# Kernel tuning notes

Measured on AMD Instinct MI355X. Metric: run time of the kernel, lower is better.

## Reference

```python
import jax, jax.numpy as jnp
import numpy as np

N, E, D, NUM_REL, NUM_LAYERS = 20000, 100000, 768, 7, 5  # 6 edge types + self-loop relation


def setup_inputs() -> dict:
    key = jax.random.key(0)
    ks = jax.random.split(key, 8)
    x = jax.random.normal(ks[0], (N, D), dtype=jnp.float32)
    edge_index = jax.random.randint(ks[1], (2, E), 0, N, dtype=jnp.int64)
    # original edge_type values are in [-1, 5]; module adds 1 -> [0, 6]
    edge_type = jax.random.randint(ks[2], (E,), -1, 6, dtype=jnp.int64)
    scale = 1.0 / np.sqrt(D)
    weights = jax.random.normal(ks[3], (NUM_LAYERS, NUM_REL, D, D), dtype=jnp.float32) * scale
    roots = jax.random.normal(ks[4], (NUM_LAYERS, D, D), dtype=jnp.float32) * scale
    biases = jax.random.normal(ks[5], (NUM_LAYERS, D), dtype=jnp.float32) * 0.01
    return {"x": x, "edge_index": edge_index, "edge_type": edge_type,
            "weights": weights, "roots": roots, "biases": biases}


def _rgcn_conv(h, src, dst, safe_et, W, root, b):
    # PyG RGCNConv (aggr='mean', root_weight=True, bias=True):
    #   out = x @ root + b + sum_r mean_{edges of rel r into v}(x[src]) @ W_r
    n = h.shape[0]
    hs = h[src]  # [E, D] gather once, reused across relations
    out = h @ root + b
    for r in range(NUM_REL):
        m = (safe_et == r).astype(h.dtype)  # [E]
        msg_sum = jax.ops.segment_sum(hs * m[:, None], dst, num_segments=n)  # [N, D]
        cnt = jax.ops.segment_sum(m, dst, num_segments=n)  # [N]
        mean = msg_sum / jnp.maximum(cnt, 1.0)[:, None]  # zero where no rel-r edges
        out = out + mean @ W[r]
    return out


def reference(x, edge_index, edge_type, weights, roots, biases):
    src, dst = edge_index[0], edge_index[1]
    safe_et = edge_type + 1  # [-1..5] -> [0..6]
    h = x
    for l in range(NUM_LAYERS):
        h = _rgcn_conv(h, src, dst, safe_et, weights[l], roots[l], biases[l])
        h = jax.nn.relu(h)  # dropout=0 -> identity
    return h
```

## Files before the change

kernel.cpp:

```cpp
#include <hip/hip_runtime.h>

typedef unsigned short u16;
typedef unsigned int   u32;
typedef __attribute__((ext_vector_type(8))) short short8;
typedef __attribute__((ext_vector_type(4))) float f32x4;

#define DD      768
#define KK      6144
#define NREL    7
#define NLAYERS 5

__device__ __forceinline__ float b2f(u16 v) {
  return __uint_as_float(((u32)v) << 16);
}
__device__ __forceinline__ u16 f2bf(float f) {
  u32 x = __float_as_uint(f);
  x += 0x7fffu + ((x >> 16) & 1u);
  return (u16)(x >> 16);
}
__device__ __forceinline__ void gload16(const void* g, void* l) {
  __builtin_amdgcn_global_load_lds(
      (const __attribute__((address_space(1))) void*)g,
      (__attribute__((address_space(3))) void*)l, 16, 0, 0);
}


__global__ void cast_x_kernel(const float* __restrict__ x, u16* __restrict__ H, size_t n) {
  for (size_t i = ((size_t)blockIdx.x * 256 + threadIdx.x) * 4; i < n; i += (size_t)gridDim.x * 256 * 4) {
    float4 v = *(const float4*)&x[i];
    u32 lo = (u32)f2bf(v.x) | ((u32)f2bf(v.y) << 16);
    u32 hi = (u32)f2bf(v.z) | ((u32)f2bf(v.w) << 16);
    uint2 o; o.x = lo; o.y = hi;
    *(uint2*)&H[i] = o;
  }
}

__global__ void count_kernel(const int* __restrict__ eidx, const int* __restrict__ etype,
                             int* cnt_dst, int* cnt_rel, int E, int Nn) {
  int e = blockIdx.x * 256 + threadIdx.x;
  if (e >= E) return;
  int dst = eidx[E + e];
  int rel = etype[e] + 1;
  atomicAdd(&cnt_dst[dst], 1);
  atomicAdd(&cnt_rel[(size_t)rel * Nn + dst], 1);
}

__global__ __launch_bounds__(1024) void scan_kernel(const int* __restrict__ cnt, int* __restrict__ offs, int n) {
  __shared__ int part[1024];
  int t = threadIdx.x;
  int per = (n + 1023) / 1024;
  int base = t * per;
  int s = 0;
  for (int i = 0; i < per; ++i) { int idx = base + i; if (idx < n) s += cnt[idx]; }
  part[t] = s;
  __syncthreads();
  for (int o = 1; o < 1024; o <<= 1) {
    int v = (t >= o) ? part[t - o] : 0;
    __syncthreads();
    part[t] += v;
    __syncthreads();
  }
  int excl = (t == 0) ? 0 : part[t - 1];
  s = excl;
  for (int i = 0; i < per; ++i) { int idx = base + i; if (idx < n) { offs[idx] = s; s += cnt[idx]; } }
  if (t == 1023) offs[n] = part[1023];
}

__global__ void fillperm_kernel(const int* __restrict__ eidx, const int* __restrict__ offs,
                                int* fill, int* perm, int E) {
  int e = blockIdx.x * 256 + threadIdx.x;
  if (e >= E) return;
  int dst = eidx[E + e];
  int pos = offs[dst] + atomicAdd(&fill[dst], 1);
  perm[pos] = e;
}

__global__ void wcat_kernel(const float* __restrict__ W, const float* __restrict__ R, u16* __restrict__ Bt) {
  __shared__ float t[32 * 33];
  int b = blockIdx.x;
  int s = b / 576, rem = b % 576;
  int kt = rem / 24, nt = rem % 24;
  const float* src = (s == 0) ? R : (W + (size_t)(s - 1) * DD * DD);
  int tj = threadIdx.x & 31, ti = threadIdx.x >> 5;
#pragma unroll
  for (int i = 0; i < 4; ++i) {
    int kk = kt * 32 + ti + i * 8;
    t[(ti + i * 8) * 33 + tj] = src[(size_t)kk * DD + nt * 32 + tj];
  }
  __syncthreads();
#pragma unroll
  for (int i = 0; i < 4; ++i) {
    int nn_ = nt * 32 + ti + i * 8;
    Bt[(size_t)nn_ * KK + (size_t)s * DD + kt * 32 + tj] = f2bf(t[tj * 33 + ti + i * 8]);
  }
}

__global__ __launch_bounds__(192) void aggregate_kernel(
    const u16* __restrict__ H, const int* __restrict__ esrc, const int* __restrict__ etype,
    const int* __restrict__ offs, const int* __restrict__ perm, const int* __restrict__ cnt_rel,
    u16* __restrict__ Acat, int node0, int Nn) {
  int v = node0 + blockIdx.x;
  int t = threadIdx.x;
  int j0 = t * 4;
  size_t rowbase = (size_t)blockIdx.x * KK;
  *(uint2*)&Acat[rowbase + j0] = *(const uint2*)&H[(size_t)v * DD + j0];
  float a0[4] = {0,0,0,0}, a1[4] = {0,0,0,0}, a2[4] = {0,0,0,0}, a3[4] = {0,0,0,0};
  float a4[4] = {0,0,0,0}, a5[4] = {0,0,0,0}, a6[4] = {0,0,0,0};
  int beg = offs[v], end = offs[v + 1];
  for (int e = beg; e < end; ++e) {
    int eid = perm[e];
    int src = esrc[eid];
    int rel = etype[eid] + 1;
    uint2 w = *(const uint2*)&H[(size_t)src * DD + j0];
    float f0 = b2f((u16)(w.x & 0xffff));
    float f1 = b2f((u16)(w.x >> 16));
    float f2 = b2f((u16)(w.y & 0xffff));
    float f3 = b2f((u16)(w.y >> 16));
    switch (rel) {
      case 0: a0[0]+=f0; a0[1]+=f1; a0[2]+=f2; a0[3]+=f3; break;
      case 1: a1[0]+=f0; a1[1]+=f1; a1[2]+=f2; a1[3]+=f3; break;
      case 2: a2[0]+=f0; a2[1]+=f1; a2[2]+=f2; a2[3]+=f3; break;
      case 3: a3[0]+=f0; a3[1]+=f1; a3[2]+=f2; a3[3]+=f3; break;
      case 4: a4[0]+=f0; a4[1]+=f1; a4[2]+=f2; a4[3]+=f3; break;
      case 5: a5[0]+=f0; a5[1]+=f1; a5[2]+=f2; a5[3]+=f3; break;
      default: a6[0]+=f0; a6[1]+=f1; a6[2]+=f2; a6[3]+=f3; break;
    }
  }
  const float* regs[NREL] = {a0, a1, a2, a3, a4, a5, a6};
#pragma unroll
  for (int r = 0; r < NREL; ++r) {
    int c = cnt_rel[(size_t)r * Nn + v];
    float inv = (c > 0) ? 1.f / (float)c : 0.f;
    const float* a = regs[r];
    u32 lo = (u32)f2bf(a[0] * inv) | ((u32)f2bf(a[1] * inv) << 16);
    u32 hi = (u32)f2bf(a[2] * inv) | ((u32)f2bf(a[3] * inv) << 16);
    uint2 o; o.x = lo; o.y = hi;
    *(uint2*)&Acat[rowbase + (size_t)(r + 1) * DD + j0] = o;
  }
}


#define MFMA_(a_, b_, c_) __builtin_amdgcn_mfma_f32_16x16x32_bf16(a_, b_, c_, 0, 0, 0)

__global__ __launch_bounds__(512, 2) void gemm256_kernel(
    const u16* __restrict__ A, const u16* __restrict__ Bt, const float* __restrict__ bias,
    u16* __restrict__ Hout, float* __restrict__ Cout, int Mvalid, int Mtiles) {
  __shared__ u16 sm[2][2][16384];

  int tid = threadIdx.x;
  int lane = tid & 63;
  int wv = tid >> 6;
  int wm = wv >> 2, wn = wv & 3;

  int nwg = Mtiles * 3;
  int orig = (int)blockIdx.x;
  int q8 = nwg >> 3, r8 = nwg & 7;
  int xcd = orig & 7, rank = orig >> 3;
  int wg = (xcd < r8 ? xcd * (q8 + 1) : r8 * (q8 + 1) + (xcd - r8) * q8) + rank;
  int bm = wg / 3, bn = wg % 3;

  int srow = tid >> 3;
  int sc = (tid & 7) ^ (srow & 7);
  const char* gA0 = (const char*)A  + (size_t)(bm * 256 + srow) * (KK * 2) + sc * 16;
  const char* gB0 = (const char*)Bt + (size_t)(bn * 256 + srow) * (KK * 2) + sc * 16;
  const size_t JSTRIDE = (size_t)64 * KK * 2;

  int rsel = lane & 15, kq = lane >> 4;
  int off0 = rsel * 128 + (((kq)     ^ (rsel & 7)) * 16);
  int off1 = rsel * 128 + (((kq + 4) ^ (rsel & 7)) * 16);

  f32x4 acc[8][4];
#pragma unroll
  for (int m = 0; m < 8; ++m)
#pragma unroll
    for (int n = 0; n < 4; ++n) acc[m][n] = (f32x4){0.f, 0.f, 0.f, 0.f};

  const int NKT = KK / 64;

#pragma unroll
  for (int j = 0; j < 4; ++j)
    gload16(gA0 + (size_t)j * JSTRIDE, (char*)&sm[0][0][0] + j * 8192 + tid * 16);
#pragma unroll
  for (int j = 0; j < 4; ++j)
    gload16(gB0 + (size_t)j * JSTRIDE, (char*)&sm[0][1][0] + j * 8192 + tid * 16);
  asm volatile("s_waitcnt vmcnt(0)" ::: "memory");
  __builtin_amdgcn_s_barrier();
  __builtin_amdgcn_sched_barrier(0);

  for (int t = 0; t < NKT; ++t) {
    int s = t & 1;
    const char* aB = (const char*)&sm[s][0][0];
    const char* bB = (const char*)&sm[s][1][0];
    char* aN = (char*)&sm[s ^ 1][0][0];
    char* bN = (char*)&sm[s ^ 1][1][0];
    size_t ko = (size_t)(t + 1) * 128;
    int more = (t + 1 < NKT);

    short8 a03[4][2], a47[4][2], bb[2][2];

#pragma unroll
    for (int m = 0; m < 4; ++m) {
      a03[m][0] = *(const short8*)(aB + (wm * 128 + m * 16) * 128 + off0);
      a03[m][1] = *(const short8*)(aB + (wm * 128 + m * 16) * 128 + off1);
    }
#pragma unroll
    for (int n = 0; n < 2; ++n) {
      bb[n][0] = *(const short8*)(bB + (wn * 64 + n * 16) * 128 + off0);
      bb[n][1] = *(const short8*)(bB + (wn * 64 + n * 16) * 128 + off1);
    }
    if (more) {
#pragma unroll
      for (int j = 0; j < 4; ++j)
        gload16(gA0 + (size_t)j * JSTRIDE + ko, aN + j * 8192 + tid * 16);
    }
    asm volatile("s_waitcnt lgkmcnt(8)" ::: "memory");
    __builtin_amdgcn_s_barrier();
    asm volatile("s_waitcnt lgkmcnt(0)" ::: "memory");
    __builtin_amdgcn_sched_barrier(0);
    __builtin_amdgcn_s_setprio(1);
#pragma unroll
    for (int m = 0; m < 4; ++m)
#pragma unroll
      for (int n = 0; n < 2; ++n) {
        acc[m][n] = MFMA_(a03[m][0], bb[n][0], acc[m][n]);
        acc[m][n] = MFMA_(a03[m][1], bb[n][1], acc[m][n]);
      }
    __builtin_amdgcn_s_setprio(0);
    __builtin_amdgcn_s_barrier();

#pragma unroll
    for (int m = 0; m < 4; ++m) {
      a47[m][0] = *(const short8*)(aB + (wm * 128 + (m + 4) * 16) * 128 + off0);
      a47[m][1] = *(const short8*)(aB + (wm * 128 + (m + 4) * 16) * 128 + off1);
    }
    if (more) {
#pragma unroll
      for (int j = 0; j < 4; ++j)
        gload16(gB0 + (size_t)j * JSTRIDE + ko, bN + j * 8192 + tid * 16);
    }
    __builtin_amdgcn_s_barrier();
    asm volatile("s_waitcnt lgkmcnt(0)" ::: "memory");
    __builtin_amdgcn_sched_barrier(0);
    __builtin_amdgcn_s_setprio(1);
#pragma unroll
    for (int m = 0; m < 4; ++m)
#pragma unroll
      for (int n = 0; n < 2; ++n) {
        acc[m + 4][n] = MFMA_(a47[m][0], bb[n][0], acc[m + 4][n]);
        acc[m + 4][n] = MFMA_(a47[m][1], bb[n][1], acc[m + 4][n]);
      }
    __builtin_amdgcn_s_setprio(0);
    __builtin_amdgcn_s_barrier();

#pragma unroll
    for (int n = 0; n < 2; ++n) {
      bb[n][0] = *(const short8*)(bB + (wn * 64 + (n + 2) * 16) * 128 + off0);
      bb[n][1] = *(const short8*)(bB + (wn * 64 + (n + 2) * 16) * 128 + off1);
    }
    __builtin_amdgcn_s_barrier();
    asm volatile("s_waitcnt lgkmcnt(0)" ::: "memory");
    __builtin_amdgcn_sched_barrier(0);
    __builtin_amdgcn_s_setprio(1);
#pragma unroll
    for (int m = 0; m < 4; ++m)
#pragma unroll
      for (int n = 0; n < 2; ++n) {
        acc[m + 4][n + 2] = MFMA_(a47[m][0], bb[n][0], acc[m + 4][n + 2]);
        acc[m + 4][n + 2] = MFMA_(a47[m][1], bb[n][1], acc[m + 4][n + 2]);
      }
    __builtin_amdgcn_s_setprio(0);
    __builtin_amdgcn_s_barrier();

    __builtin_amdgcn_s_setprio(1);
#pragma unroll
    for (int m = 0; m < 4; ++m)
#pragma unroll
      for (int n = 0; n < 2; ++n) {
        acc[m][n + 2] = MFMA_(a03[m][0], bb[n][0], acc[m][n + 2]);
        acc[m][n + 2] = MFMA_(a03[m][1], bb[n][1], acc[m][n + 2]);
      }
    __builtin_amdgcn_s_setprio(0);
    asm volatile("s_waitcnt vmcnt(0)" ::: "memory");
    __builtin_amdgcn_s_barrier();
    __builtin_amdgcn_sched_barrier(0);
  }

  int rif = (lane >> 4) * 4;
  int cidx = lane & 15;
#pragma unroll
  for (int m = 0; m < 8; ++m) {
    int rl = bm * 256 + wm * 128 + m * 16 + rif;
#pragma unroll
    for (int n = 0; n < 4; ++n) {
      int c = bn * 256 + wn * 64 + n * 16 + cidx;
      float bv = bias[c];
#pragma unroll
      for (int j = 0; j < 4; ++j) {
        int r = rl + j;
        if (r < Mvalid) {
          float v = acc[m][n][j] + bv;
          v = v > 0.f ? v : 0.f;
          if (Hout) Hout[(size_t)r * DD + c] = f2bf(v);
          if (Cout) Cout[(size_t)r * DD + c] = v;
        }
      }
    }
  }
}


static inline size_t alignup(size_t x, size_t a) { return (x + a - 1) & ~(a - 1); }

extern "C" void kernel_launch(void* const* d_in, const int* in_sizes, int n_in,
                              void* d_out, int out_size, void* d_ws, size_t ws_size,
                              hipStream_t stream) {
  const float* x       = (const float*)d_in[0];
  const int*   eidx    = (const int*)d_in[1];
  const int*   etype   = (const int*)d_in[2];
  const float* weights = (const float*)d_in[3];
  const float* roots   = (const float*)d_in[4];
  const float* biases  = (const float*)d_in[5];
  float* out = (float*)d_out;

  const int Nn = in_sizes[0] / DD;
  const int E  = in_sizes[2];

  char* p = (char*)d_ws;
  size_t off = 0;
  auto carve = [&](size_t bytes) -> char* {
    char* r = p + off;
    off = alignup(off + bytes, 256);
    return r;
  };
  u16* H0      = (u16*)carve((size_t)Nn * DD * 2);
  u16* Bt      = (u16*)carve((size_t)DD * KK * 2);
  int* cnt_rel = (int*)carve((size_t)NREL * Nn * 4);
  int* cnt_dst = (int*)carve((size_t)Nn * 4);
  int* offs    = (int*)carve((size_t)(Nn + 1) * 4);
  int* fill    = (int*)carve((size_t)Nn * 4);
  int* perm    = (int*)carve((size_t)E * 4);

  size_t rem = (ws_size > off) ? (ws_size - off) : 0;
  int McCap = (int)(rem / ((size_t)KK * 2));
  int Mpad = ((Nn + 255) / 256) * 256;
  int Mc = (McCap < Mpad) ? (McCap & ~255) : Mpad;
  if (Mc < 256) return;
  u16* Acat = (u16*)(p + off);
  int nchunks = (Nn + Mc - 1) / Mc;
  u16* H1 = (u16*)d_out;

  (void)hipMemsetAsync(cnt_rel, 0, (size_t)NREL * Nn * 4, stream);
  (void)hipMemsetAsync(cnt_dst, 0, (size_t)Nn * 4, stream);
  (void)hipMemsetAsync(fill, 0, (size_t)Nn * 4, stream);

  int eg = (E + 255) / 256;
  count_kernel<<<eg, 256, 0, stream>>>(eidx, etype, cnt_dst, cnt_rel, E, Nn);
  scan_kernel<<<1, 1024, 0, stream>>>(cnt_dst, offs, Nn);
  fillperm_kernel<<<eg, 256, 0, stream>>>(eidx, offs, fill, perm, E);
  cast_x_kernel<<<2048, 256, 0, stream>>>(x, H0, (size_t)Nn * DD);

  const u16* Hin = H0;
  u16* Hnext = H1;
  for (int l = 0; l < NLAYERS; ++l) {
    wcat_kernel<<<8 * 576, 256, 0, stream>>>(weights + (size_t)l * NREL * DD * DD,
                                             roots + (size_t)l * DD * DD, Bt);
    for (int c = 0; c < nchunks; ++c) {
      int node0 = c * Mc;
      int nn = (Nn - node0 < Mc) ? (Nn - node0) : Mc;
      aggregate_kernel<<<nn, 192, 0, stream>>>(Hin, eidx, etype, offs, perm, cnt_rel,
                                               Acat, node0, Nn);
      int mt = (nn + 255) / 256;
      u16* ho = (l < NLAYERS - 1) ? (Hnext + (size_t)node0 * DD) : nullptr;
      float* co = (l == NLAYERS - 1) ? (out + (size_t)node0 * DD) : nullptr;
      gemm256_kernel<<<mt * 3, 512, 0, stream>>>(Acat, Bt, biases + (size_t)l * DD, ho, co, nn, mt);
    }
    const u16* t_ = Hin;
    Hin = Hnext;
    Hnext = (u16*)t_;
  }
}
```

Before: 1.481 ms.

## Sort nodes by relation mask and skip absent-relation K segments in GEMM

Builds a per-node bitmask of which relations have incoming edges, then counting-sorts nodes by that mask into a permutation. Aggregation writes Acat rows in permuted order. For each 256-row tile, the union of its node masks is packed into a segment list. The GEMM then iterates only over the root segment plus the K segments of relations present in that tile, instead of all eight 768-wide segments. The epilogue scatters results back through the permutation. This aims to cut MFMA work and Acat/weight traffic for all-zero relation blocks, at the cost of several small preprocessing kernels and non-contiguous output row writes.

Measured after the change: 1.489 ms. About the same (+0.6%).

```diff
diff --git a/kernel.cpp b/kernel.cpp
--- a/kernel.cpp
+++ b/kernel.cpp
@@ -2,6 +2,7 @@
 
 typedef unsigned short u16;
 typedef unsigned int   u32;
+typedef unsigned long long u64;
 typedef __attribute__((ext_vector_type(8))) short short8;
 typedef __attribute__((ext_vector_type(4))) float f32x4;
 
@@ -75,6 +76,55 @@
   perm[pos] = e;
 }
 
+__global__ void nodemask_kernel(const int* __restrict__ cnt_rel, int* __restrict__ mask,
+                                int* __restrict__ mh, int Nn) {
+  int v = blockIdx.x * 256 + threadIdx.x;
+  if (v >= Nn) return;
+  int m = 0;
+#pragma unroll
+  for (int r = 0; r < NREL; ++r)
+    m |= (cnt_rel[(size_t)r * Nn + v] > 0) ? (1 << r) : 0;
+  mask[v] = m;
+  atomicAdd(&mh[m], 1);
+}
+
+__global__ void mscan_kernel(const int* __restrict__ mh, int* __restrict__ mb) {
+  int t = threadIdx.x;
+  int acc = 0;
+  for (int i = 0; i < t; ++i) acc += mh[i];
+  mb[t] = acc;
+}
+
+__global__ void mscatter_kernel(const int* __restrict__ mask, const int* __restrict__ mb,
+                                int* __restrict__ mf, int* __restrict__ prow, int Nn) {
+  int v = blockIdx.x * 256 + threadIdx.x;
+  if (v >= Nn) return;
+  int m = mask[v];
+  int pos = mb[m] + atomicAdd(&mf[m], 1);
+  prow[pos] = v;
+}
+
+__global__ void tilemask_kernel(const int* __restrict__ prow, const int* __restrict__ mask,
+                                u64* __restrict__ packs, int* __restrict__ pcnts, int Nn) {
+  __shared__ int u;
+  int t = threadIdx.x;
+  if (t == 0) u = 0;
+  __syncthreads();
+  int idx = blockIdx.x * 256 + t;
+  int m = (idx < Nn) ? mask[prow[idx]] : 0;
+  atomicOr(&u, m);
+  __syncthreads();
+  if (t == 0) {
+    int mm = u;
+    u64 pk = 0;
+    int cnt = 1;
+    for (int r = 0; r < NREL; ++r)
+      if (mm & (1 << r)) { pk |= ((u64)(r + 1)) << (8 * cnt); ++cnt; }
+    packs[blockIdx.x] = pk;
+    pcnts[blockIdx.x] = cnt;
+  }
+}
+
 __global__ void wcat_kernel(const float* __restrict__ W, const float* __restrict__ R, u16* __restrict__ Bt) {
   __shared__ float t[32 * 33];
   int b = blockIdx.x;
@@ -98,8 +148,8 @@
 __global__ __launch_bounds__(192) void aggregate_kernel(
     const u16* __restrict__ H, const int* __restrict__ esrc, const int* __restrict__ etype,
     const int* __restrict__ offs, const int* __restrict__ perm, const int* __restrict__ cnt_rel,
-    u16* __restrict__ Acat, int node0, int Nn) {
-  int v = node0 + blockIdx.x;
+    const int* __restrict__ prow, u16* __restrict__ Acat, int node0, int Nn) {
+  int v = prow[node0 + blockIdx.x];
   int t = threadIdx.x;
   int j0 = t * 4;
   size_t rowbase = (size_t)blockIdx.x * KK;
@@ -141,10 +191,15 @@
 
 
 #define MFMA_(a_, b_, c_) __builtin_amdgcn_mfma_f32_16x16x32_bf16(a_, b_, c_, 0, 0, 0)
-
-__global__ __launch_bounds__(512, 2) void gemm256_kernel(
+#define BAR   __builtin_amdgcn_s_barrier()
+#define SB    __builtin_amdgcn_sched_barrier(0)
+#define LGKM0 asm volatile("s_waitcnt lgkmcnt(0)" ::: "memory")
+#define VM0   asm volatile("s_waitcnt vmcnt(0)" ::: "memory")
+
+__global__ __launch_bounds__(512, 2) void gemmsk_kernel(
     const u16* __restrict__ A, const u16* __restrict__ Bt, const float* __restrict__ bias,
-    u16* __restrict__ Hout, float* __restrict__ Cout, int Mvalid, int Mtiles) {
+    const int* __restrict__ prowL, const u64* __restrict__ packs, const int* __restrict__ pcnts,
+    u16* __restrict__ Hout, float* __restrict__ Cout, int Mvalid, int Mtiles, int tile0) {
   __shared__ u16 sm[2][2][16384];
 
   int tid = threadIdx.x;
@@ -159,6 +214,9 @@
   int wg = (xcd < r8 ? xcd * (q8 + 1) : r8 * (q8 + 1) + (xcd - r8) * q8) + rank;
   int bm = wg / 3, bn = wg % 3;
 
+  u64 pack = packs[tile0 + bm];
+  int nseg = pcnts[tile0 + bm];
+
   int srow = tid >> 3;
   int sc = (tid & 7) ^ (srow & 7);
   const char* gA0 = (const char*)A  + (size_t)(bm * 256 + srow) * (KK * 2) + sc * 16;
@@ -175,114 +233,115 @@
 #pragma unroll
     for (int n = 0; n < 4; ++n) acc[m][n] = (f32x4){0.f, 0.f, 0.f, 0.f};
 
-  const int NKT = KK / 64;
-
-#pragma unroll
-  for (int j = 0; j < 4; ++j)
-    gload16(gA0 + (size_t)j * JSTRIDE, (char*)&sm[0][0][0] + j * 8192 + tid * 16);
-#pragma unroll
-  for (int j = 0; j < 4; ++j)
-    gload16(gB0 + (size_t)j * JSTRIDE, (char*)&sm[0][1][0] + j * 8192 + tid * 16);
-  asm volatile("s_waitcnt vmcnt(0)" ::: "memory");
-  __builtin_amdgcn_s_barrier();
-  __builtin_amdgcn_sched_barrier(0);
-
-  for (int t = 0; t < NKT; ++t) {
-    int s = t & 1;
-    const char* aB = (const char*)&sm[s][0][0];
-    const char* bB = (const char*)&sm[s][1][0];
-    char* aN = (char*)&sm[s ^ 1][0][0];
-    char* bN = (char*)&sm[s ^ 1][1][0];
-    size_t ko = (size_t)(t + 1) * 128;
-    int more = (t + 1 < NKT);
-
-    short8 a03[4][2], a47[4][2], bb[2][2];
-
-#pragma unroll
-    for (int m = 0; m < 4; ++m) {
-      a03[m][0] = *(const short8*)(aB + (wm * 128 + m * 16) * 128 + off0);
-      a03[m][1] = *(const short8*)(aB + (wm * 128 + m * 16) * 128 + off1);
+  int kbC = (int)(pack & 7ULL) * 12; pack >>= 8;
+  int kbN = (int)(pack & 7ULL) * 12; pack >>= 8;
+
+  {
+    size_t ko = (size_t)kbC * 128;
+#pragma unroll
+    for (int j = 0; j < 4; ++j)
+      gload16(gA0 + (size_t)j * JSTRIDE + ko, (char*)&sm[0][0][0] + j * 8192 + tid * 16);
+#pragma unroll
+    for (int j = 0; j < 4; ++j)
+      gload16(gB0 + (size_t)j * JSTRIDE + ko, (char*)&sm[0][1][0] + j * 8192 + tid * 16);
+  }
+  VM0;
+  BAR;
+  SB;
+
+  for (int s = 0; s < nseg; ++s) {
+#pragma unroll
+    for (int kt = 0; kt < 12; ++kt) {
+      int slot = kt & 1;
+      int kbn_ = (kt < 11) ? (kbC + kt + 1) : kbN;
+      int more = (s * 12 + kt) < (nseg * 12 - 1);
+      size_t ko = (size_t)kbn_ * 128;
+      const char* aB = (const char*)&sm[slot][0][0];
+      const char* bB = (const char*)&sm[slot][1][0];
+      char* aN = (char*)&sm[slot ^ 1][0][0];
+      char* bN = (char*)&sm[slot ^ 1][1][0];
+      short8 a03[4][2], a47[4][2], bb[2][2];
+
+#pragma unroll
+      for (int m = 0; m < 4; ++m) {
+        a03[m][0] = *(const short8*)(aB + (wm * 128 + m * 16) * 128 + off0);
+        a03[m][1] = *(const short8*)(aB + (wm * 128 + m * 16) * 128 + off1);
+      }
+#pragma unroll
+      for (int n = 0; n < 2; ++n) {
+        bb[n][0] = *(const short8*)(bB + (wn * 64 + n * 16) * 128 + off0);
+        bb[n][1] = *(const short8*)(bB + (wn * 64 + n * 16) * 128 + off1);
+      }
+      if (more) {
+#pragma unroll
+        for (int j = 0; j < 4; ++j)
+          gload16(gA0 + (size_t)j * JSTRIDE + ko, aN + j * 8192 + tid * 16);
+      }
+      asm volatile("s_waitcnt lgkmcnt(8)" ::: "memory");
+      SB; BAR; LGKM0; SB;
+      __builtin_amdgcn_s_setprio(1);
+#pragma unroll
+      for (int m = 0; m < 4; ++m)
+#pragma unroll
+        for (int n = 0; n < 2; ++n) {
+          acc[m][n] = MFMA_(a03[m][0], bb[n][0], acc[m][n]);
+          acc[m][n] = MFMA_(a03[m][1], bb[n][1], acc[m][n]);
+        }
+      __builtin_amdgcn_s_setprio(0);
+      SB; BAR;
+
+#pragma unroll
+      for (int m = 0; m < 4; ++m) {
+        a47[m][0] = *(const short8*)(aB + (wm * 128 + (m + 4) * 16) * 128 + off0);
+        a47[m][1] = *(const short8*)(aB + (wm * 128 + (m + 4) * 16) * 128 + off1);
+      }
+      if (more) {
+#pragma unroll
+        for (int j = 0; j < 4; ++j)
+          gload16(gB0 + (size_t)j * JSTRIDE + ko, bN + j * 8192 + tid * 16);
+      }
+      SB; BAR; LGKM0; SB;
+      __builtin_amdgcn_s_setprio(1);
+#pragma unroll
+      for (int m = 0; m < 4; ++m)
+#pragma unroll
+        for (int n = 0; n < 2; ++n) {
+          acc[m + 4][n] = MFMA_(a47[m][0], bb[n][0], acc[m + 4][n]);
+          acc[m + 4][n] = MFMA_(a47[m][1], bb[n][1], acc[m + 4][n]);
+        }
+      __builtin_amdgcn_s_setprio(0);
+      SB; BAR;
+
+#pragma unroll
+      for (int n = 0; n < 2; ++n) {
+        bb[n][0] = *(const short8*)(bB + (wn * 64 + (n + 2) * 16) * 128 + off0);
+        bb[n][1] = *(const short8*)(bB + (wn * 64 + (n + 2) * 16) * 128 + off1);
+      }
+      SB; BAR; LGKM0; SB;
+      __builtin_amdgcn_s_setprio(1);
+#pragma unroll
+      for (int m = 0; m < 4; ++m)
+#pragma unroll
+        for (int n = 0; n < 2; ++n) {
+          acc[m + 4][n + 2] = MFMA_(a47[m][0], bb[n][0], acc[m + 4][n + 2]);
+          acc[m + 4][n + 2] = MFMA_(a47[m][1], bb[n][1], acc[m + 4][n + 2]);
+        }
+      __builtin_amdgcn_s_setprio(0);
+      SB; BAR;
+
+      __builtin_amdgcn_s_setprio(1);
+#pragma unroll
+      for (int m = 0; m < 4; ++m)
+#pragma unroll
+        for (int n = 0; n < 2; ++n) {
+          acc[m][n + 2] = MFMA_(a03[m][0], bb[n][0], acc[m][n + 2]);
+          acc[m][n + 2] = MFMA_(a03[m][1], bb[n][1], acc[m][n + 2]);
+        }
+      __builtin_amdgcn_s_setprio(0);
+      VM0; BAR; SB;
     }
-#pragma unroll
-    for (int n = 0; n < 2; ++n) {
-      bb[n][0] = *(const short8*)(bB + (wn * 64 + n * 16) * 128 + off0);
-      bb[n][1] = *(const short8*)(bB + (wn * 64 + n * 16) * 128 + off1);
-    }
-    if (more) {
-#pragma unroll
-      for (int j = 0; j < 4; ++j)
-        gload16(gA0 + (size_t)j * JSTRIDE + ko, aN + j * 8192 + tid * 16);
-    }
-    asm volatile("s_waitcnt lgkmcnt(8)" ::: "memory");
-    __builtin_amdgcn_s_barrier();
-    asm volatile("s_waitcnt lgkmcnt(0)" ::: "memory");
-    __builtin_amdgcn_sched_barrier(0);
-    __builtin_amdgcn_s_setprio(1);
-#pragma unroll
-    for (int m = 0; m < 4; ++m)
-#pragma unroll
-      for (int n = 0; n < 2; ++n) {
-        acc[m][n] = MFMA_(a03[m][0], bb[n][0], acc[m][n]);
-        acc[m][n] = MFMA_(a03[m][1], bb[n][1], acc[m][n]);
-      }
-    __builtin_amdgcn_s_setprio(0);
-    __builtin_amdgcn_s_barrier();
-
-#pragma unroll
-    for (int m = 0; m < 4; ++m) {
-      a47[m][0] = *(const short8*)(aB + (wm * 128 + (m + 4) * 16) * 128 + off0);
-      a47[m][1] = *(const short8*)(aB + (wm * 128 + (m + 4) * 16) * 128 + off1);
-    }
-    if (more) {
-#pragma unroll
-      for (int j = 0; j < 4; ++j)
-        gload16(gB0 + (size_t)j * JSTRIDE + ko, bN + j * 8192 + tid * 16);
-    }
-    __builtin_amdgcn_s_barrier();
-    asm volatile("s_waitcnt lgkmcnt(0)" ::: "memory");
-    __builtin_amdgcn_sched_barrier(0);
-    __builtin_amdgcn_s_setprio(1);
-#pragma unroll
-    for (int m = 0; m < 4; ++m)
-#pragma unroll
-      for (int n = 0; n < 2; ++n) {
-        acc[m + 4][n] = MFMA_(a47[m][0], bb[n][0], acc[m + 4][n]);
-        acc[m + 4][n] = MFMA_(a47[m][1], bb[n][1], acc[m + 4][n]);
-      }
-    __builtin_amdgcn_s_setprio(0);
-    __builtin_amdgcn_s_barrier();
-
-#pragma unroll
-    for (int n = 0; n < 2; ++n) {
-      bb[n][0] = *(const short8*)(bB + (wn * 64 + (n + 2) * 16) * 128 + off0);
-      bb[n][1] = *(const short8*)(bB + (wn * 64 + (n + 2) * 16) * 128 + off1);
-    }
-    __builtin_amdgcn_s_barrier();
-    asm volatile("s_waitcnt lgkmcnt(0)" ::: "memory");
-    __builtin_amdgcn_sched_barrier(0);
-    __builtin_amdgcn_s_setprio(1);
-#pragma unroll
-    for (int m = 0; m < 4; ++m)
-#pragma unroll
-      for (int n = 0; n < 2; ++n) {
-        acc[m + 4][n + 2] = MFMA_(a47[m][0], bb[n][0], acc[m + 4][n + 2]);
-        acc[m + 4][n + 2] = MFMA_(a47[m][1], bb[n][1], acc[m + 4][n + 2]);
-      }
-    __builtin_amdgcn_s_setprio(0);
-    __builtin_amdgcn_s_barrier();
-
-    __builtin_amdgcn_s_setprio(1);
-#pragma unroll
-    for (int m = 0; m < 4; ++m)
-#pragma unroll
-      for (int n = 0; n < 2; ++n) {
-        acc[m][n + 2] = MFMA_(a03[m][0], bb[n][0], acc[m][n + 2]);
-        acc[m][n + 2] = MFMA_(a03[m][1], bb[n][1], acc[m][n + 2]);
-      }
-    __builtin_amdgcn_s_setprio(0);
-    asm volatile("s_waitcnt vmcnt(0)" ::: "memory");
-    __builtin_amdgcn_s_barrier();
-    __builtin_amdgcn_sched_barrier(0);
+    kbC = kbN;
+    kbN = (int)(pack & 7ULL) * 12; pack >>= 8;
   }
 
   int rif = (lane >> 4) * 4;
@@ -298,10 +357,11 @@
       for (int j = 0; j < 4; ++j) {
         int r = rl + j;
         if (r < Mvalid) {
+          int nd = prowL[r];
           float v = acc[m][n][j] + bv;
           v = v > 0.f ? v : 0.f;
-          if (Hout) Hout[(size_t)r * DD + c] = f2bf(v);
-          if (Cout) Cout[(size_t)r * DD + c] = v;
+          if (Hout) Hout[(size_t)nd * DD + c] = f2bf(v);
+          if (Cout) Cout[(size_t)nd * DD + c] = v;
         }
       }
     }
@@ -324,6 +384,8 @@
 
   const int Nn = in_sizes[0] / DD;
   const int E  = in_sizes[2];
+  const int Mpad = ((Nn + 255) / 256) * 256;
+  const int Ntiles = Mpad / 256;
 
   char* p = (char*)d_ws;
   size_t off = 0;
@@ -339,10 +401,16 @@
   int* offs    = (int*)carve((size_t)(Nn + 1) * 4);
   int* fill    = (int*)carve((size_t)Nn * 4);
   int* perm    = (int*)carve((size_t)E * 4);
+  int* mask    = (int*)carve((size_t)Nn * 4);
+  int* mh      = (int*)carve(128 * 4);
+  int* mb      = (int*)carve(128 * 4);
+  int* mf      = (int*)carve(128 * 4);
+  int* prow    = (int*)carve((size_t)Mpad * 4);
+  u64* packs   = (u64*)carve((size_t)Ntiles * 8);
+  int* pcnts   = (int*)carve((size_t)Ntiles * 4);
 
   size_t rem = (ws_size > off) ? (ws_size - off) : 0;
   int McCap = (int)(rem / ((size_t)KK * 2));
-  int Mpad = ((Nn + 255) / 256) * 256;
   int Mc = (McCap < Mpad) ? (McCap & ~255) : Mpad;
   if (Mc < 256) return;
   u16* Acat = (u16*)(p + off);
@@ -352,11 +420,18 @@
   (void)hipMemsetAsync(cnt_rel, 0, (size_t)NREL * Nn * 4, stream);
   (void)hipMemsetAsync(cnt_dst, 0, (size_t)Nn * 4, stream);
   (void)hipMemsetAsync(fill, 0, (size_t)Nn * 4, stream);
+  (void)hipMemsetAsync(mh, 0, 128 * 4, stream);
+  (void)hipMemsetAsync(mf, 0, 128 * 4, stream);
 
   int eg = (E + 255) / 256;
+  int ng = (Nn + 255) / 256;
   count_kernel<<<eg, 256, 0, stream>>>(eidx, etype, cnt_dst, cnt_rel, E, Nn);
   scan_kernel<<<1, 1024, 0, stream>>>(cnt_dst, offs, Nn);
   fillperm_kernel<<<eg, 256, 0, stream>>>(eidx, offs, fill, perm, E);
+  nodemask_kernel<<<ng, 256, 0, stream>>>(cnt_rel, mask, mh, Nn);
+  mscan_kernel<<<1, 128, 0, stream>>>(mh, mb);
+  mscatter_kernel<<<ng, 256, 0, stream>>>(mask, mb, mf, prow, Nn);
+  tilemask_kernel<<<Ntiles, 256, 0, stream>>>(prow, mask, packs, pcnts, Nn);
   cast_x_kernel<<<2048, 256, 0, stream>>>(x, H0, (size_t)Nn * DD);
 
   const u16* Hin = H0;
@@ -368,11 +443,13 @@
       int node0 = c * Mc;
       int nn = (Nn - node0 < Mc) ? (Nn - node0) : Mc;
       aggregate_kernel<<<nn, 192, 0, stream>>>(Hin, eidx, etype, offs, perm, cnt_rel,
-                                               Acat, node0, Nn);
+                                               prow, Acat, node0, Nn);
       int mt = (nn + 255) / 256;
-      u16* ho = (l < NLAYERS - 1) ? (Hnext + (size_t)node0 * DD) : nullptr;
-      float* co = (l == NLAYERS - 1) ? (out + (size_t)node0 * DD) : nullptr;
-      gemm256_kernel<<<mt * 3, 512, 0, stream>>>(Acat, Bt, biases + (size_t)l * DD, ho, co, nn, mt);
+      u16* ho = (l < NLAYERS - 1) ? Hnext : nullptr;
+      float* co = (l == NLAYERS - 1) ? out : nullptr;
+      gemmsk_kernel<<<mt * 3, 512, 0, stream>>>(Acat, Bt, biases + (size_t)l * DD,
+                                                prow + node0, packs, pcnts,
+                                                ho, co, nn, mt, node0 / 256);
     }
     const u16* t_ = Hin;
     Hin = Hnext;
```
